# Optimization experiments

Measured on AMD Instinct MI355X. Metric: run time of the kernel, lower is better.

## Reference

```python
import jax, jax.numpy as jnp
import numpy as np

B, S, D, G, N_ORIG = 4, 4096, 512, 64, 4096
EPS_NORM = 1e-12   # F.normalize eps
EPS_MERGE = 1e-8   # merge-weight eps


def setup_inputs() -> dict:
    key = jax.random.key(0)
    k1, k2, k3 = jax.random.split(key, 3)
    x = jax.random.normal(k1, (B, S, D), dtype=jnp.float32)
    source = jax.random.uniform(k2, (B, S, N_ORIG), dtype=jnp.float32)
    position_ids = jnp.arange(B * S, dtype=jnp.int64).reshape(B, S)
    W = jax.random.normal(k3, (D, G), dtype=jnp.float32) * 0.05  # group_proj weight (no bias)
    return {"x": x, "source": source, "position_ids": position_ids,
            "r": 1024, "window_size": 16, "W": W}


def _token_merge(x, source, position_ids, r, window_size, W):
    Bb, Ss, Dd = x.shape
    r = min(r, Ss // 2)
    idx = jnp.arange(Ss, dtype=jnp.int32)
    # local candidate pairs: |i-j| = d for d in 1..window_size-1
    pi = jnp.concatenate([idx[:Ss - d] for d in range(1, min(window_size, Ss))])
    pj = jnp.concatenate([idx[d:] for d in range(1, min(window_size, Ss))])

    g = x @ W                                   # (B,S,G)
    norms = jnp.linalg.norm(g, axis=-1)         # (B,S)
    gn = g / jnp.maximum(norms, EPS_NORM)[..., None]
    sim = jnp.einsum('bpg,bpg->bp', gn[:, pi], gn[:, pj])  # (B,P)

    def greedy(sim_b):
        # deterministic order: score DESC, i ASC, j ASC
        order = jnp.lexsort((pj, pi, -sim_b))
        oi, oj = pi[order], pj[order]

        def step(carry, ij):
            used, partner, cnt = carry
            i, j = ij
            take = (cnt < r) & (~used[i]) & (~used[j])
            used = used.at[i].set(used[i] | take).at[j].set(used[j] | take)
            partner = partner.at[i].set(jnp.where(take, j, partner[i]))
            cnt = cnt + take.astype(jnp.int32)
            return (used, partner, cnt), None

        init = (jnp.zeros(Ss, bool), jnp.full(Ss, -1, jnp.int32), jnp.int32(0))
        (used, partner, cnt), _ = jax.lax.scan(step, init, (oi, oj))
        return partner  # partner[i] = j if pair (i,j) selected, else -1

    partner = jax.vmap(greedy)(sim)  # (B,S)

    def merge(xb, sb, pb, partner_b, norms_b):
        sel = partner_b >= 0
        pj_safe = jnp.where(sel, partner_b, idx)
        wi = norms_b
        wj = jnp.where(sel, norms_b[pj_safe], 0.0)
        merged = (wi[:, None] * xb + wj[:, None] * xb[pj_safe]) / (wi + wj + EPS_MERGE)[:, None]
        x_m = jnp.where(sel[:, None], merged, xb)
        s_m = sb + jnp.where(sel, 1.0, 0.0)[:, None] * sb[pj_safe]
        # drop the second token of each merged pair, preserving order
        skip_idx = jnp.where(sel, partner_b, Ss)
        skip = jnp.zeros(Ss, bool).at[skip_idx].set(True, mode='drop')
        keep = jnp.argsort(skip.astype(jnp.int8), stable=True)[: Ss - r]
        return x_m[keep], s_m[keep], pb[keep]

    return jax.vmap(merge)(x, source, position_ids, partner, norms)


def reference(x, source, position_ids, r, window_size, W):
    return _token_merge(x, source, position_ids, r, window_size, W)
```

## Files before the change

### kernel.cpp

```cpp
#include <hip/hip_runtime.h>

#define BATCH 4
#define SLEN 4096
#define DDIM 512
#define GDIM 64
#define NORIG 4096
#define WMAX 15
#define RSEL 1024
#define KEEP (SLEN - RSEL)
#define NTOK (BATCH * SLEN)
#define PEEL_ROUNDS 256
#define LDSL 32

typedef float __attribute__((ext_vector_type(4))) f32x4;

#define OFF_LISTS ((size_t)0)
#define OFF_GN    ((size_t)0)
#define OFF_SIMST ((size_t)8388608)
#define OFF_NORMS ((size_t)10485760)
#define OFF_KT    ((size_t)10584064)
#define OFF_PJR   ((size_t)10633216)
#define OFF_WIR   ((size_t)10682368)
#define OFF_WJR   ((size_t)10731520)
#define WS_NEEDED ((size_t)10780672)

#define OUTX_OFF 0
#define OUTS_OFF 6291456
#define OUTP_OFF 56623104

__global__ __launch_bounds__(256) void k_proj(const float* __restrict__ x,
                                              const float* __restrict__ Wm,
                                              double* __restrict__ gn,
                                              float* __restrict__ norms) {
  __shared__ float xs[16 * DDIM];
  int base = blockIdx.x * 16;
  const float4* src = (const float4*)(x + (size_t)base * DDIM);
  float4* dstv = (float4*)xs;
  for (int idx = threadIdx.x; idx < 16 * DDIM / 4; idx += 256) dstv[idx] = src[idx];
  __syncthreads();
  int lane = threadIdx.x & 63;
  int wv = threadIdx.x >> 6;
  double acc0 = 0, acc1 = 0, acc2 = 0, acc3 = 0;
  const float* xw = xs + wv * 4 * DDIM;
  for (int d = 0; d < DDIM; ++d) {
    double wval = (double)Wm[d * GDIM + lane];
    acc0 += (double)xw[d] * wval;
    acc1 += (double)xw[DDIM + d] * wval;
    acc2 += (double)xw[2 * DDIM + d] * wval;
    acc3 += (double)xw[3 * DDIM + d] * wval;
  }
  double accs[4] = {acc0, acc1, acc2, acc3};
  for (int k = 0; k < 4; ++k) {
    double a = accs[k];
    double ss = a * a;
    for (int o = 32; o >= 1; o >>= 1) ss += __shfl_xor(ss, o, 64);
    double nrm = sqrt(ss);
    int tok = base + wv * 4 + k;
    if (lane == 0) norms[tok] = (float)nrm;
    double denom = nrm > 1e-12 ? nrm : 1e-12;
    gn[(size_t)tok * GDIM + lane] = a / denom;
  }
}

__global__ __launch_bounds__(256) void k_sims(const double* __restrict__ gn,
                                              double* __restrict__ simsT) {
  int blk = blockIdx.x;
  int b = blk >> 6;
  int t0 = (blk & 63) * 64;
  int nrows = min(64 + WMAX, SLEN - t0);
  __shared__ double gs[(64 + WMAX) * GDIM];
  const double* src = gn + ((size_t)b * SLEN + t0) * GDIM;
  for (int idx = threadIdx.x; idx < nrows * GDIM; idx += 256) gs[idx] = src[idx];
  __syncthreads();
  int lane = threadIdx.x & 63, wv = threadIdx.x >> 6;
  for (int s = wv; s < 64 * WMAX; s += 4) {
    int il = s & 63, d = (s >> 6) + 1;
    int i = t0 + il;
    if (i + d < SLEN) {
      double p = gs[il * GDIM + lane] * gs[(il + d) * GDIM + lane];
      for (int o = 32; o >= 1; o >>= 1) p += __shfl_xor(p, o, 64);
      if (lane == 0) simsT[((size_t)(b * SLEN + i)) * 16 + d] = p;
    }
  }
}

__global__ __launch_bounds__(256) void k_lists(const double* __restrict__ simsT,
                                               signed char* __restrict__ lists8) {
  __shared__ signed char stage[4][32];
  int wave = threadIdx.x >> 6, lane = threadIdx.x & 63;
  int t = blockIdx.x * 4 + wave;
  int b = t >> 12, tt = t & (SLEN - 1);
  const double* sb = simsT + (size_t)b * SLEN * 16;
  int d = (lane >> 1) + 1;
  int side = lane & 1;
  bool valid = (lane < 30) && (side == 0 ? (tt + d < SLEN) : (tt - d >= 0));
  unsigned long long key = 0ULL;
  unsigned int code = 0xFFFFu;
  signed char delta = 0;
  if (valid) {
    int i = (side == 0) ? tt : (tt - d);
    double s = sb[(size_t)i * 16 + d];
    unsigned long long bits = (unsigned long long)__double_as_longlong(s);
    key = (bits & 0x8000000000000000ULL) ? ~bits : (bits | 0x8000000000000000ULL);
    code = (unsigned int)((i << 4) | d);
    delta = (side == 0) ? (signed char)d : (signed char)(-d);
  }
  int rank = 0;
#pragma clang loop unroll(disable)
  for (int q = 0; q < 30; ++q) {
    unsigned long long kq = __shfl(key, q, 64);
    unsigned int cq = __shfl(code, q, 64);
    if (kq != 0ULL && (kq > key || (kq == key && cq < code))) rank++;
  }
  if (lane < 32) stage[wave][lane] = 0;
  if (valid) stage[wave][rank] = delta;
  if (lane < 32) lists8[(size_t)t * 32 + lane] = stage[wave][lane];
}

__global__ __launch_bounds__(1024) void k_match(const signed char* __restrict__ lists8,
                                                const double* __restrict__ simsT_all,
                                                const float* __restrict__ norms,
                                                int* __restrict__ kt, int* __restrict__ pjr,
                                                float* __restrict__ wir, float* __restrict__ wjr,
                                                float* __restrict__ out_pos) {
  int b = blockIdx.x;
  const signed char* lb = lists8 + (size_t)b * SLEN * 32;
  const double* simsT = simsT_all + (size_t)b * SLEN * 16;
  __shared__ __align__(16) unsigned char big[SLEN * LDSL];
  __shared__ __align__(8) signed char bp[SLEN];
  __shared__ unsigned char usedA[SLEN];
  __shared__ unsigned char cur[SLEN];
  __shared__ unsigned short takenCode[2048];
  __shared__ unsigned char meta[SLEN];
  __shared__ int takenCnt, baseCnt;
  __shared__ int sharedB, sharedNeed, sdone, allAccept, smallStraddle;
  __shared__ int memberCnt;
  __shared__ int wTot[16], wOff[16];
  signed char* l8 = (signed char*)big;
  int tid = threadIdx.x;

#pragma clang loop unroll(disable)
  for (int t = tid; t < SLEN; t += 1024) {
    const unsigned long long* lp = (const unsigned long long*)(lb + (size_t)t * 32);
    unsigned long long v0 = lp[0], v1 = lp[1], v2 = lp[2], v3 = lp[3];
    unsigned long long* dp = (unsigned long long*)(l8 + t * LDSL);
    dp[0] = v0; dp[1] = v1; dp[2] = v2; dp[3] = v3;
    bp[t] = (signed char)(v0 & 0xFF);
    usedA[t] = 0; cur[t] = 0; meta[t] = 0;
  }
  if (tid == 0) takenCnt = 0;
  __syncthreads();

  int tb4 = tid * 4;
#pragma clang loop unroll(disable)
  for (int round = 0; round < PEEL_ROUNDS; ++round) {
    if (tid == 0) baseCnt = takenCnt;
    __syncthreads();
    {
      unsigned int w4 = *(const unsigned int*)(bp + tb4);
      if (w4 != 0u) {
#pragma clang loop unroll(disable)
        for (int u = 0; u < 4; ++u) {
          signed char dlt = (signed char)(w4 >> (8 * u));
          if (dlt > 0) {
            int t = tb4 + u;
            int j = t + dlt;
            if (bp[j] == (signed char)(-dlt)) {
              int idx = atomicAdd(&takenCnt, 1);
              if (idx < 2048) takenCode[idx] = (unsigned short)((t << 4) | dlt);
              usedA[t] = 1; usedA[j] = 1;
            }
          }
        }
      }
    }
    __syncthreads();
    int newCnt = takenCnt;
    if (newCnt == baseCnt) break;
    {
      unsigned int w4 = *(const unsigned int*)(bp + tb4);
      if (w4 != 0u) {
#pragma clang loop unroll(disable)
        for (int u = 0; u < 4; ++u) {
          signed char dlt = (signed char)(w4 >> (8 * u));
          if (dlt == 0) continue;
          int t = tb4 + u;
          if (usedA[t]) { bp[t] = 0; continue; }
          int p = t + dlt;
          int cc = cur[t];
          bool adv = false;
#pragma clang loop unroll(disable)
          while (dlt != 0 && usedA[p]) {
            ++cc; adv = true;
            dlt = (cc < LDSL) ? l8[t * LDSL + cc] : (signed char)0;
            p = t + dlt;
          }
          if (adv) { cur[t] = (unsigned char)cc; bp[t] = dlt; }
        }
      }
    }
    __syncthreads();
  }

  unsigned long long* key = (unsigned long long*)big;
  unsigned short* codeA = (unsigned short*)(big + 16384);
  unsigned char* state = (unsigned char*)(big + 20480);
  unsigned int* hist = (unsigned int*)(big + 22528);
  unsigned int* bcum = (unsigned int*)(big + 23552);
  unsigned int* wsum = (unsigned int*)(big + 24576);
  unsigned short* memberIdx = (unsigned short*)(big + 24704);
  int m = min(takenCnt, 2048);
  __syncthreads();
#pragma clang loop unroll(disable)
  for (int k = tid; k < m; k += 1024) {
    unsigned short c = takenCode[k];
    codeA[k] = c;
    state[k] = 0;
    double s = simsT[(size_t)(c >> 4) * 16 + (c & 15)];
    unsigned long long bits = (unsigned long long)__double_as_longlong(s);
    key[k] = (bits & 0x8000000000000000ULL) ? ~bits : (bits | 0x8000000000000000ULL);
  }
  if (tid == 0) { sharedNeed = RSEL; sdone = 0; allAccept = (m <= RSEL); smallStraddle = 0; memberCnt = 0; }
  __syncthreads();

  if (!allAccept) {
#pragma clang loop unroll(disable)
    for (int pass = 0; pass < 8; ++pass) {
      if (tid < 256) hist[tid] = 0;
      __syncthreads();
      int sh = 56 - 8 * pass;
#pragma clang loop unroll(disable)
      for (int k = tid; k < m; k += 1024)
        if (!state[k]) atomicAdd(&hist[(unsigned int)(key[k] >> sh) & 0xFFu], 1u);
      __syncthreads();
      unsigned int v = 0, inc = 0;
      int lane = tid & 63, w = tid >> 6;
      if (tid < 256) {
        v = hist[255 - tid];
        inc = v;
        for (int o = 1; o < 64; o <<= 1) { unsigned int n = __shfl_up(inc, o, 64); if (lane >= o) inc += n; }
        if (lane == 63) wsum[w] = inc;
      }
      __syncthreads();
      if (tid < 256) {
        unsigned int off = 0;
        for (int ww = 0; ww < w; ++ww) off += wsum[ww];
        unsigned int incl = inc + off;
        bcum[255 - tid] = incl - v;
      }
      __syncthreads();
      if (tid < 256) {
        int bkt = 255 - tid;
        unsigned int ag = bcum[bkt];
        unsigned int need = (unsigned int)sharedNeed;
        if (ag < need && ag + hist[bkt] >= need) sharedB = bkt;
      }
      __syncthreads();
      int B = sharedB;
      unsigned int needInB = (unsigned int)sharedNeed - bcum[B];
#pragma clang loop unroll(disable)
      for (int k = tid; k < m; k += 1024) {
        if (!state[k]) {
          unsigned int bv = (unsigned int)(key[k] >> sh) & 0xFFu;
          if ((int)bv > B) state[k] = 1;
          else if ((int)bv < B) state[k] = 2;
        }
      }
      __syncthreads();
      if (tid == 0) {
        sharedNeed = (int)needInB;
        if (hist[B] == needInB) sdone = 1;
        else if (hist[B] <= 128) smallStraddle = 1;
      }
      __syncthreads();
      if (sdone || smallStraddle) break;
    }
  }
  __syncthreads();

  if (allAccept || sdone) {
#pragma clang loop unroll(disable)
    for (int k = tid; k < m; k += 1024) if (!state[k]) state[k] = 1;
  } else {
#pragma clang loop unroll(disable)
    for (int k = tid; k < m; k += 1024)
      if (!state[k]) { int idx = atomicAdd(&memberCnt, 1); memberIdx[idx] = (unsigned short)k; }
    __syncthreads();
    int mc = memberCnt;
    unsigned int need = (unsigned int)sharedNeed;
#pragma clang loop unroll(disable)
    for (int z = tid; z < mc; z += 1024) {
      int k = memberIdx[z];
      unsigned long long kk = key[k];
      unsigned short ck = codeA[k];
      unsigned int wr = 0;
#pragma clang loop unroll(disable)
      for (int q2 = 0; q2 < mc; ++q2) {
        int q = memberIdx[q2];
        unsigned long long kq = key[q];
        if (kq > kk || (kq == kk && codeA[q] < ck)) wr++;
      }
      if (wr < need) state[k] = 1;
    }
  }
  __syncthreads();
#pragma clang loop unroll(disable)
  for (int k = tid; k < m; k += 1024) {
    if (state[k] == 1) {
      unsigned short ck = codeA[k];
      int i = ck >> 4, d = ck & 15;
      meta[i] = (unsigned char)d;
      meta[i + d] = 0x80;
    }
  }
  __syncthreads();
  int cnt = 0; unsigned char kf[4];
  int tbase = tid * 4;
  for (int u = 0; u < 4; ++u) { kf[u] = (meta[tbase + u] & 0x80) ? 0 : 1; cnt += kf[u]; }
  int lane = tid & 63, wv = tid >> 6;
  int incl = cnt;
  for (int o = 1; o < 64; o <<= 1) { int n = __shfl_up(incl, o, 64); if (lane >= o) incl += n; }
  if (lane == 63) wTot[wv] = incl;
  __syncthreads();
  if (tid < 16) {
    int v2 = wTot[tid];
    for (int o = 1; o < 16; o <<= 1) { int n = __shfl_up(v2, o, 64); if (lane >= o) v2 += n; }
    wOff[tid] = v2 - wTot[tid];
  }
  __syncthreads();
  int pos = wOff[wv] + (incl - cnt);
  for (int u = 0; u < 4; ++u) {
    int t = tbase + u;
    if (kf[u]) {
      if (pos < KEEP) {
        int orow = b * KEEP + pos;
        kt[orow] = t;
        int d = meta[t] & 15;
        pjr[orow] = d ? (t + d) : -1;
        wir[orow] = norms[b * SLEN + t];
        wjr[orow] = d ? norms[b * SLEN + t + d] : 0.0f;
        out_pos[orow] = (float)(b * SLEN + t);
      }
      pos++;
    }
  }
}

__global__ __launch_bounds__(256) void k_gather(const float* __restrict__ x,
                                                const float* __restrict__ src,
                                                const int* __restrict__ kt, const int* __restrict__ pjr,
                                                const float* __restrict__ wir, const float* __restrict__ wjr,
                                                float* __restrict__ outx, float* __restrict__ outs) {
  int orow = blockIdx.x;
  int b = orow / KEEP;
  int t = kt[orow], pj = pjr[orow];
  int gi = min(max(b * SLEN + t, 0), NTOK - 1);
  int gj = min(b * SLEN + min(max(pj, 0), SLEN - 1), NTOK - 1);
  int c = threadIdx.x;
  if (c < 128) {
    const f32x4* xi = (const f32x4*)(x + (size_t)gi * DDIM);
    f32x4 v = __builtin_nontemporal_load(&xi[c]);
    if (pj >= 0) {
      const f32x4* xj = (const f32x4*)(x + (size_t)gj * DDIM);
      f32x4 u = __builtin_nontemporal_load(&xj[c]);
      float wi = wir[orow], wj = wjr[orow];
      float inv = 1.0f / (wi + wj + 1e-8f);
      v = (v * wi + u * wj) * inv;
    }
    __builtin_nontemporal_store(v, (f32x4*)(outx + (size_t)orow * DDIM) + c);
  }
  const f32x4* si = (const f32x4*)(src + (size_t)gi * NORIG);
  f32x4* o = (f32x4*)(outs + (size_t)orow * NORIG);
  if (pj >= 0) {
    const f32x4* sj = (const f32x4*)(src + (size_t)gj * NORIG);
    for (int u = 0; u < 4; ++u) {
      int c2 = c + u * 256;
      f32x4 a = __builtin_nontemporal_load(&si[c2]);
      f32x4 bb = __builtin_nontemporal_load(&sj[c2]);
      __builtin_nontemporal_store(a + bb, &o[c2]);
    }
  } else {
    for (int u = 0; u < 4; ++u) {
      int c2 = c + u * 256;
      f32x4 a = __builtin_nontemporal_load(&si[c2]);
      __builtin_nontemporal_store(a, &o[c2]);
    }
  }
}

extern "C" void kernel_launch(void* const* d_in, const int* in_sizes, int n_in,
                              void* d_out, int out_size, void* d_ws, size_t ws_size,
                              hipStream_t stream) {
  if (ws_size < WS_NEEDED) return;

  const float* x = (const float*)d_in[0];
  const float* source = (const float*)d_in[1];
  const float* Wm = (const float*)d_in[5];

  char* ws = (char*)d_ws;
  double* gn = (double*)(ws + OFF_GN);
  double* simsT = (double*)(ws + OFF_SIMST);
  float* norms = (float*)(ws + OFF_NORMS);
  signed char* lists8 = (signed char*)(ws + OFF_LISTS);
  int* kt = (int*)(ws + OFF_KT);
  int* pjr = (int*)(ws + OFF_PJR);
  float* wir = (float*)(ws + OFF_WIR);
  float* wjr = (float*)(ws + OFF_WJR);

  float* out = (float*)d_out;
  float* outx = out + OUTX_OFF;
  float* outs = out + OUTS_OFF;
  float* outp = out + OUTP_OFF;

  k_proj<<<(BATCH * SLEN) / 16, 256, 0, stream>>>(x, Wm, gn, norms);
  k_sims<<<BATCH * (SLEN / 64), 256, 0, stream>>>(gn, simsT);
  k_lists<<<NTOK / 4, 256, 0, stream>>>(simsT, lists8);
  k_match<<<BATCH, 1024, 0, stream>>>(lists8, simsT, norms, kt, pjr, wir, wjr, outp);
  k_gather<<<BATCH * KEEP, 256, 0, stream>>>(x, source, kt, pjr, wir, wjr, outx, outs);
}
```

Measured before the change: 331.5 us.

## Fuse similarity and per-token ranked-list kernels with halo recompute in LDS

```diff
diff --git a/kernel.cpp b/kernel.cpp
--- a/kernel.cpp
+++ b/kernel.cpp
@@ -18,11 +18,12 @@
 #define OFF_GN    ((size_t)0)
 #define OFF_SIMST ((size_t)8388608)
 #define OFF_NORMS ((size_t)10485760)
-#define OFF_KT    ((size_t)10584064)
-#define OFF_PJR   ((size_t)10633216)
-#define OFF_WIR   ((size_t)10682368)
-#define OFF_WJR   ((size_t)10731520)
-#define WS_NEEDED ((size_t)10780672)
+#define OFF_LISTS2 ((size_t)10551296)
+#define OFF_KT    ((size_t)11075584)
+#define OFF_PJR   ((size_t)11124736)
+#define OFF_WIR   ((size_t)11173888)
+#define OFF_WJR   ((size_t)11223040)
+#define WS_NEEDED ((size_t)11272192)
 
 #define OUTX_OFF 0
 #define OUTS_OFF 6291456
@@ -62,59 +63,68 @@
   }
 }
 
-__global__ __launch_bounds__(256) void k_sims(const double* __restrict__ gn,
-                                              double* __restrict__ simsT) {
+__global__ __launch_bounds__(256) void k_simslists(const double* __restrict__ gn,
+                                                   double* __restrict__ simsT,
+                                                   signed char* __restrict__ lists8) {
   int blk = blockIdx.x;
   int b = blk >> 6;
   int t0 = (blk & 63) * 64;
-  int nrows = min(64 + WMAX, SLEN - t0);
-  __shared__ double gs[(64 + WMAX) * GDIM];
-  const double* src = gn + ((size_t)b * SLEN + t0) * GDIM;
-  for (int idx = threadIdx.x; idx < nrows * GDIM; idx += 256) gs[idx] = src[idx];
+  int sBase = t0 - 15;
+  int gLo = max(sBase, 0);
+  int gHi = min(t0 + 78, SLEN - 1);
+  int nrows = gHi - gLo + 1;
+  __shared__ double gs[94 * GDIM];
+  __shared__ double simLDS[79 * 16];
+  __shared__ signed char stage[4][32];
+  const double* srcg = gn + ((size_t)b * SLEN + gLo) * GDIM;
+  for (int idx = threadIdx.x; idx < nrows * GDIM; idx += 256) gs[idx] = srcg[idx];
   __syncthreads();
   int lane = threadIdx.x & 63, wv = threadIdx.x >> 6;
-  for (int s = wv; s < 64 * WMAX; s += 4) {
-    int il = s & 63, d = (s >> 6) + 1;
-    int i = t0 + il;
-    if (i + d < SLEN) {
-      double p = gs[il * GDIM + lane] * gs[(il + d) * GDIM + lane];
+#pragma clang loop unroll(disable)
+  for (int s = wv; s < 79 * WMAX; s += 4) {
+    int ii = s % 79;
+    int d = s / 79 + 1;
+    int i = sBase + ii;
+    if (i >= 0 && i + d < SLEN) {
+      const double* ra = gs + (size_t)(i - gLo) * GDIM;
+      const double* rb = gs + (size_t)(i + d - gLo) * GDIM;
+      double p = ra[lane] * rb[lane];
       for (int o = 32; o >= 1; o >>= 1) p += __shfl_xor(p, o, 64);
-      if (lane == 0) simsT[((size_t)(b * SLEN + i)) * 16 + d] = p;
-    }
-  }
-}
-
-__global__ __launch_bounds__(256) void k_lists(const double* __restrict__ simsT,
-                                               signed char* __restrict__ lists8) {
-  __shared__ signed char stage[4][32];
-  int wave = threadIdx.x >> 6, lane = threadIdx.x & 63;
-  int t = blockIdx.x * 4 + wave;
-  int b = t >> 12, tt = t & (SLEN - 1);
-  const double* sb = simsT + (size_t)b * SLEN * 16;
-  int d = (lane >> 1) + 1;
-  int side = lane & 1;
-  bool valid = (lane < 30) && (side == 0 ? (tt + d < SLEN) : (tt - d >= 0));
-  unsigned long long key = 0ULL;
-  unsigned int code = 0xFFFFu;
-  signed char delta = 0;
-  if (valid) {
-    int i = (side == 0) ? tt : (tt - d);
-    double s = sb[(size_t)i * 16 + d];
-    unsigned long long bits = (unsigned long long)__double_as_longlong(s);
-    key = (bits & 0x8000000000000000ULL) ? ~bits : (bits | 0x8000000000000000ULL);
-    code = (unsigned int)((i << 4) | d);
-    delta = (side == 0) ? (signed char)d : (signed char)(-d);
-  }
-  int rank = 0;
-#pragma clang loop unroll(disable)
-  for (int q = 0; q < 30; ++q) {
-    unsigned long long kq = __shfl(key, q, 64);
-    unsigned int cq = __shfl(code, q, 64);
-    if (kq != 0ULL && (kq > key || (kq == key && cq < code))) rank++;
-  }
-  if (lane < 32) stage[wave][lane] = 0;
-  if (valid) stage[wave][rank] = delta;
-  if (lane < 32) lists8[(size_t)t * 32 + lane] = stage[wave][lane];
+      if (lane == 0) {
+        simLDS[ii * 16 + d] = p;
+        if (i >= t0) simsT[((size_t)(b * SLEN + i)) * 16 + d] = p;
+      }
+    }
+  }
+  __syncthreads();
+#pragma clang loop unroll(disable)
+  for (int it = 0; it < 16; ++it) {
+    int tt = t0 + wv * 16 + it;
+    int d = (lane >> 1) + 1;
+    int side = lane & 1;
+    bool valid = (lane < 30) && (side == 0 ? (tt + d < SLEN) : (tt - d >= 0));
+    unsigned long long key = 0ULL;
+    unsigned int code = 0xFFFFu;
+    signed char delta = 0;
+    if (valid) {
+      int i = (side == 0) ? tt : (tt - d);
+      double s = simLDS[(i - sBase) * 16 + d];
+      unsigned long long bits = (unsigned long long)__double_as_longlong(s);
+      key = (bits & 0x8000000000000000ULL) ? ~bits : (bits | 0x8000000000000000ULL);
+      code = (unsigned int)((i << 4) | d);
+      delta = (side == 0) ? (signed char)d : (signed char)(-d);
+    }
+    int rank = 0;
+#pragma clang loop unroll(disable)
+    for (int q = 0; q < 30; ++q) {
+      unsigned long long kq = __shfl(key, q, 64);
+      unsigned int cq = __shfl(code, q, 64);
+      if (kq != 0ULL && (kq > key || (kq == key && cq < code))) rank++;
+    }
+    if (lane < 32) stage[wv][lane] = 0;
+    if (valid) stage[wv][rank] = delta;
+    if (lane < 32) lists8[(size_t)(b * SLEN + tt) * 32 + lane] = stage[wv][lane];
+  }
 }
 
 __global__ __launch_bounds__(1024) void k_match(const signed char* __restrict__ lists8,
@@ -401,7 +411,7 @@
   double* gn = (double*)(ws + OFF_GN);
   double* simsT = (double*)(ws + OFF_SIMST);
   float* norms = (float*)(ws + OFF_NORMS);
-  signed char* lists8 = (signed char*)(ws + OFF_LISTS);
+  signed char* lists8 = (signed char*)(ws + OFF_LISTS2);
   int* kt = (int*)(ws + OFF_KT);
   int* pjr = (int*)(ws + OFF_PJR);
   float* wir = (float*)(ws + OFF_WIR);
@@ -413,8 +423,7 @@
   float* outp = out + OUTP_OFF;
 
   k_proj<<<(BATCH * SLEN) / 16, 256, 0, stream>>>(x, Wm, gn, norms);
-  k_sims<<<BATCH * (SLEN / 64), 256, 0, stream>>>(gn, simsT);
-  k_lists<<<NTOK / 4, 256, 0, stream>>>(simsT, lists8);
+  k_simslists<<<BATCH * (SLEN / 64), 256, 0, stream>>>(gn, simsT, lists8);
   k_match<<<BATCH, 1024, 0, stream>>>(lists8, simsT, norms, kt, pjr, wir, wjr, outp);
   k_gather<<<BATCH * KEEP, 256, 0, stream>>>(x, source, kt, pjr, wir, wjr, outx, outs);
 }
```

After: 408.6 us. +23.3%, slower.
